# Optimization experiments

Hardware: AMD Instinct MI355X
Metric: run time of the kernel (lower is better)

The kernel has to match this reference:

```python
import jax, jax.numpy as jnp
import numpy as np

B, N, KD, VD, ID, H = 2, 2048, 1024, 1024, 1024, 16
HD = ID // H
SCALE = ID ** (-0.5)  # module quirk: scale uses inner_dim, not head_dim
EPS = 1e-5


def layernorm(x, g, b):
    mu = jnp.mean(x, axis=-1, keepdims=True)
    var = jnp.var(x, axis=-1, keepdims=True)
    return (x - mu) * jax.lax.rsqrt(var + EPS) * g + b


def setup_inputs() -> dict:
    key = jax.random.key(0)
    ks = jax.random.split(key, 12)
    d = {
        "keys": jax.random.normal(ks[0], (B, N, KD), jnp.float32),
        "values": jax.random.normal(ks[1], (B, N, VD), jnp.float32),
        "qk_norm_g": jnp.ones((KD,), jnp.float32),
        "qk_norm_b": jnp.zeros((KD,), jnp.float32),
        "value_norm_g": jnp.ones((VD,), jnp.float32),
        "value_norm_b": jnp.zeros((VD,), jnp.float32),
        "key_norm_g": jnp.ones((ID,), jnp.float32),
        "key_norm_b": jnp.zeros((ID,), jnp.float32),
        "query_norm_g": jnp.ones((ID,), jnp.float32),
        "query_norm_b": jnp.zeros((ID,), jnp.float32),
        "w_qk": jax.random.normal(ks[2], (KD, 2 * ID), jnp.float32) * (KD ** -0.5),
        "w_v": jax.random.normal(ks[3], (VD, ID), jnp.float32) * (VD ** -0.5),
        "w_out": jax.random.normal(ks[4], (ID, VD), jnp.float32) * (ID ** -0.5),
        "b_out": jnp.zeros((VD,), jnp.float32),
    }
    return d


def reference(keys, values, qk_norm_g, qk_norm_b, value_norm_g, value_norm_b,
              key_norm_g, key_norm_b, query_norm_g, query_norm_b,
              w_qk, w_v, w_out, b_out):
    keys = layernorm(keys, qk_norm_g, qk_norm_b)
    values = layernorm(values, value_norm_g, value_norm_b)
    qk = keys @ w_qk  # [B,N,2*ID]
    q, k = qk[..., :ID], qk[..., ID:]
    q = layernorm(q, query_norm_g, query_norm_b)
    k = layernorm(k, key_norm_g, key_norm_b)
    # b n (h d) -> b h n d
    q = q.reshape(B, N, H, HD).transpose(0, 2, 1, 3)
    k = k.reshape(B, N, H, HD).transpose(0, 2, 1, 3)
    v = (values @ w_v).reshape(B, N, H, HD).transpose(0, 2, 1, 3)
    dots = jnp.einsum('bhqd,bhkd->bhqk', q, k) * SCALE
    attn = jax.nn.softmax(dots, axis=-1)
    out = jnp.einsum('bhqk,bhkd->bhqd', attn, v)
    out = out.transpose(0, 2, 1, 3).reshape(B, N, ID)
    return out @ w_out + b_out
```

## Files before the change

kernel.cpp:

```cpp
#include <hip/hip_runtime.h>
#include <hip/hip_bf16.h>
#include <type_traits>


typedef __hip_bfloat16 bf16;
typedef __attribute__((ext_vector_type(8))) short bf16x8;
typedef __attribute__((ext_vector_type(4))) float f32x4;

#define MFMA_BF16(a, b, c) __builtin_amdgcn_mfma_f32_16x16x32_bf16((a), (b), (c), 0, 0, 0)

__device__ __forceinline__ float us2f(unsigned short u) {
  unsigned int v = ((unsigned int)u) << 16;
  return __builtin_bit_cast(float, v);
}

__device__ __forceinline__ unsigned pack_bf16x2(float a, float b) {
  union { __hip_bfloat162 h; unsigned u; } cv;
  cv.h = __float22bfloat162_rn(float2{a, b});
  return cv.u;
}

__device__ __forceinline__ unsigned pack_bf16x2_trunc(float a, float b) {
  return __builtin_amdgcn_perm(__builtin_bit_cast(unsigned, b),
                               __builtin_bit_cast(unsigned, a), 0x07060302u);
}

__device__ __forceinline__ void gl_lds16(const bf16* g, bf16* l) {
  __builtin_amdgcn_global_load_lds(
      (const __attribute__((address_space(1))) void*)g,
      (__attribute__((address_space(3))) void*)l, 16, 0, 0);
}

__device__ __forceinline__ void barrier_pinned() {
  __builtin_amdgcn_s_barrier();
  __builtin_amdgcn_sched_barrier(0);
}

template <typename TIN>
__device__ __forceinline__ void ln_core(
    const TIN* __restrict__ in, const float* __restrict__ gamma,
    const float* __restrict__ beta, bf16* __restrict__ out,
    int stride, int D, float sc, int row, float* red)
{
  const int t = threadIdx.x;
  float x0, x1, x2, x3;
  if constexpr (std::is_same_v<TIN, float>) {
    float4 u = *(const float4*)(in + (size_t)row * stride + t * 4);
    x0 = u.x; x1 = u.y; x2 = u.z; x3 = u.w;
  } else {
    ushort4 u = *(const ushort4*)(in + (size_t)row * stride + t * 4);
    x0 = us2f(u.x); x1 = us2f(u.y); x2 = us2f(u.z); x3 = us2f(u.w);
  }
  float s = x0 + x1 + x2 + x3;
  float s2 = x0 * x0 + x1 * x1 + x2 * x2 + x3 * x3;
#pragma unroll
  for (int m = 1; m < 64; m <<= 1) {
    s += __shfl_xor(s, m);
    s2 += __shfl_xor(s2, m);
  }
  const int w = t >> 6, lane = t & 63;
  if (lane == 0) { red[w] = s; red[4 + w] = s2; }
  __syncthreads();
  if (t == 0) {
    float S = red[0] + red[1] + red[2] + red[3];
    float S2 = red[4] + red[5] + red[6] + red[7];
    float mu = S / (float)D;
    float var = S2 / (float)D - mu * mu;
    red[8] = mu;
    red[9] = rsqrtf(var + 1e-5f);
  }
  __syncthreads();
  const float mu = red[8], rs = red[9];
  float4 g4 = *(const float4*)(gamma + t * 4);
  float4 b4 = *(const float4*)(beta + t * 4);
  uint2 o;
  o.x = pack_bf16x2(((x0 - mu) * rs * g4.x + b4.x) * sc, ((x1 - mu) * rs * g4.y + b4.y) * sc);
  o.y = pack_bf16x2(((x2 - mu) * rs * g4.z + b4.z) * sc, ((x3 - mu) * rs * g4.w + b4.w) * sc);
  *(uint2*)(out + (size_t)row * D + t * 4) = o;
}

template <typename TIN>
__global__ __launch_bounds__(256) void ln2_kernel(
    const TIN* __restrict__ in0, const TIN* __restrict__ in1, int stride,
    const float* __restrict__ g0, const float* __restrict__ b0,
    const float* __restrict__ g1, const float* __restrict__ b1,
    bf16* __restrict__ out0, bf16* __restrict__ out1, int D,
    float sc0, float sc1)
{
  __shared__ float red[10];
  const int which = blockIdx.y;
  ln_core<TIN>(which ? in1 : in0, which ? g1 : g0, which ? b1 : b0,
               which ? out1 : out0, stride, D, which ? sc1 : sc0,
               blockIdx.x, red);
}

__device__ __forceinline__ void transpose_core(
    const float* __restrict__ in, bf16* __restrict__ out, int C,
    int r0, int c0, float (*tile)[68])
{
  const int R = 1024;
  const int t = threadIdx.x;
  const int lr = t >> 2, lc = (t & 3) * 16;
  const float* src = in + (size_t)(r0 + lr) * C + (c0 + lc);
#pragma unroll
  for (int i = 0; i < 4; ++i) {
    float4 u = *(const float4*)(src + i * 4);
    tile[lr][lc + i * 4 + 0] = u.x;
    tile[lr][lc + i * 4 + 1] = u.y;
    tile[lr][lc + i * 4 + 2] = u.z;
    tile[lr][lc + i * 4 + 3] = u.w;
  }
  __syncthreads();
  __align__(16) bf16 tmp[16];
#pragma unroll
  for (int j = 0; j < 16; ++j) tmp[j] = __float2bfloat16(tile[lc + j][lr]);
  bf16* dst = out + (size_t)(c0 + lr) * R + (r0 + lc);
  *(bf16x8*)dst       = *(const bf16x8*)&tmp[0];
  *(bf16x8*)(dst + 8) = *(const bf16x8*)&tmp[8];
}

__global__ __launch_bounds__(256) void prep_kernel(
    const float* __restrict__ keys, const float* __restrict__ values,
    const float* __restrict__ qk_g, const float* __restrict__ qk_b,
    const float* __restrict__ val_g, const float* __restrict__ val_b,
    bf16* __restrict__ keys_ln, bf16* __restrict__ values_ln,
    const float* __restrict__ w_qk, bf16* __restrict__ wqkT,
    const float* __restrict__ w_v, bf16* __restrict__ wvT,
    const float* __restrict__ w_out, bf16* __restrict__ woutT)
{
  __shared__ float tile[64][68];
  __shared__ float red[10];
  const int bid = blockIdx.x;
  if (bid < 8192) {
    const int row = bid >> 1, which = bid & 1;
    ln_core<float>(which ? values : keys, which ? val_g : qk_g,
                   which ? val_b : qk_b, which ? values_ln : keys_ln,
                   1024, 1024, 1.0f, row, red);
  } else {
    const int tz = bid - 8192;
    if (tz < 512) {
      transpose_core(w_qk, wqkT, 2048, (tz >> 5) * 64, (tz & 31) * 64, tile);
    } else if (tz < 768) {
      const int s = tz - 512;
      transpose_core(w_v, wvT, 1024, (s >> 4) * 64, (s & 15) * 64, tile);
    } else {
      const int s = tz - 768;
      transpose_core(w_out, woutT, 1024, (s >> 4) * 64, (s & 15) * 64, tile);
    }
  }
}

template <int BM, int BN, int TMODE, typename TOUT>
__device__ __forceinline__ void gemm_core(
    const bf16* __restrict__ A, const bf16* __restrict__ Bt,
    const float* __restrict__ bias, TOUT* __restrict__ C,
    int N, int K, int has_bias, int bx, int by, bf16* smem)
{
  constexpr int MT = BM / 32, NT = BN / 32;
  constexpr int ASL = BM / 32, BSL = BN / 32;
  constexpr int BUFE = (BM + BN) * 64;
  const int t = threadIdx.x;
  const int w = t >> 6, lane = t & 63, l15 = lane & 15, quad = lane >> 4;
  const int wy = w >> 1, wx = w & 1;
  const bf16* Ab = A + (size_t)by * BM * K;
  const bf16* Bb = Bt + (size_t)bx * BN * K;
  f32x4 acc[MT][NT] = {};

  const bf16* aptr[ASL];
  const bf16* bptr[BSL];
#pragma unroll
  for (int i = 0; i < ASL; ++i) {
    int s = i * 256 + t, row = s >> 3, c = (s & 7) ^ (row & 7);
    aptr[i] = Ab + (size_t)row * K + (c << 3);
  }
#pragma unroll
  for (int i = 0; i < BSL; ++i) {
    int s = i * 256 + t, row = s >> 3, c = (s & 7) ^ (row & 7);
    bptr[i] = Bb + (size_t)row * K + (c << 3);
  }

  auto stage = [&](bf16* buf, int kc) {
#pragma unroll
    for (int i = 0; i < ASL; ++i)
      gl_lds16(aptr[i] + kc, buf + (i * 256 + t) * 8);
#pragma unroll
    for (int i = 0; i < BSL; ++i)
      gl_lds16(bptr[i] + kc, buf + BM * 64 + (i * 256 + t) * 8);
  };

  const int sw = (quad ^ (l15 & 7)) << 3;
  const int NK = K >> 6;

  stage(smem, 0);

  for (int kt = 0; kt < NK; ++kt) {
    const int cur = kt & 1;
    bf16* lA = smem + cur * BUFE;
    bf16* lB = lA + BM * 64;
    barrier_pinned();
    if (kt + 1 < NK) {
      stage(smem + (cur ^ 1) * BUFE, (kt + 1) << 6);
      if constexpr (ASL + BSL == 8)
        asm volatile("s_waitcnt vmcnt(8)" ::: "memory");
      else
        asm volatile("s_waitcnt vmcnt(6)" ::: "memory");
    } else {
      asm volatile("s_waitcnt vmcnt(0)" ::: "memory");
    }
    barrier_pinned();

#pragma unroll
    for (int h = 0; h < 2; ++h) {
      const int so = sw ^ (h << 5);
      bf16x8 af[MT], bfr[NT];
#pragma unroll
      for (int mt = 0; mt < MT; ++mt)
        af[mt] = *(const bf16x8*)&lA[(wy * (BM / 2) + mt * 16 + l15) * 64 + so];
#pragma unroll
      for (int nt = 0; nt < NT; ++nt)
        bfr[nt] = *(const bf16x8*)&lB[(wx * (BN / 2) + nt * 16 + l15) * 64 + so];
#pragma unroll
      for (int mt = 0; mt < MT; ++mt)
#pragma unroll
        for (int nt = 0; nt < NT; ++nt)
          acc[mt][nt] = MFMA_BF16(af[mt], bfr[nt], acc[mt][nt]);
    }
  }

  if constexpr (TMODE == 1) {
    constexpr int STR = BM + 8;
    static_assert(BN * STR <= 2 * BUFE, "lOut must fit staging buffers");
    bf16* lOut = smem;
    __syncthreads();
#pragma unroll
    for (int mt = 0; mt < MT; ++mt)
#pragma unroll
      for (int nt = 0; nt < NT; ++nt) {
        const int d = wx * (BN / 2) + nt * 16 + l15;
        const int n = wy * (BM / 2) + mt * 16 + quad * 4;
        uint2 pk;
        pk.x = pack_bf16x2(acc[mt][nt][0], acc[mt][nt][1]);
        pk.y = pack_bf16x2(acc[mt][nt][2], acc[mt][nt][3]);
        *(uint2*)&lOut[d * STR + n] = pk;
      }
    __syncthreads();
    const int row0 = by * BM;
    const int bidx = row0 >> 11, n0 = row0 & 2047;
    const int col0 = bx * BN;
    constexpr int CPR = BM / 32;
    constexpr int NITER = (BN * CPR) / 256;
#pragma unroll
    for (int it = 0; it < NITER; ++it) {
      const int idx = it * 256 + t;
      const int d = idx / CPR, off = (idx % CPR) * 32;
      const bf16* srcp = &lOut[d * STR + off];
      bf16* g = (bf16*)C + ((size_t)(bidx << 10) + col0 + d) * 2048 + n0 + off;
#pragma unroll
      for (int j = 0; j < 4; ++j)
        *(bf16x8*)(g + j * 8) = *(const bf16x8*)(srcp + j * 8);
    }
  } else {
    const int row_base = by * BM + wy * (BM / 2);
    const int col_base = bx * BN + wx * (BN / 2);
#pragma unroll
    for (int mt = 0; mt < MT; ++mt)
#pragma unroll
      for (int nt = 0; nt < NT; ++nt) {
        const int col = col_base + nt * 16 + l15;
        const float bb = has_bias ? bias[col] : 0.0f;
#pragma unroll
        for (int r = 0; r < 4; ++r) {
          const int row = row_base + mt * 16 + quad * 4 + r;
          float v = acc[mt][nt][r] + bb;
          if constexpr (std::is_same_v<TOUT, bf16>)
            C[(size_t)row * N + col] = __float2bfloat16(v);
          else
            C[(size_t)row * N + col] = v;
        }
      }
  }
}

template <int BM, int BN, int TMODE, typename TOUT>
__global__ __launch_bounds__(256) void gemm_bt_kernel(
    const bf16* __restrict__ A, const bf16* __restrict__ Bt,
    const float* __restrict__ bias, TOUT* __restrict__ C,
    int N, int K, int has_bias)
{
  __shared__ __align__(16) bf16 smem[2 * (BM + BN) * 64];
  gemm_core<BM, BN, TMODE, TOUT>(A, Bt, bias, C, N, K, has_bias,
                                 blockIdx.x, blockIdx.y, smem);
}

__global__ __launch_bounds__(256) void gemm_dual_kernel(
    const bf16* __restrict__ A0, const bf16* __restrict__ B0, bf16* __restrict__ C0,
    const bf16* __restrict__ A1, const bf16* __restrict__ B1, bf16* __restrict__ C1)
{
  __shared__ __align__(16) bf16 smem[2 * 256 * 64];
  const int bid = blockIdx.x;
  if (bid < 512) {
    gemm_core<128, 128, 0, bf16>(A0, B0, nullptr, C0, 2048, 1024, 0,
                                 bid & 15, bid >> 4, smem);
  } else {
    const int b = bid - 512;
    gemm_core<128, 128, 1, bf16>(A1, B1, nullptr, C1, 1024, 1024, 0,
                                 b & 7, b >> 3, smem);
  }
}

__global__ __launch_bounds__(256) void flash_kernel(
    const bf16* __restrict__ Q, const bf16* __restrict__ Km,
    const bf16* __restrict__ Vt, bf16* __restrict__ O)
{
  __shared__ __align__(16) bf16 smem[8192 + 8192 + 8192];
  bf16* lQ = smem;
  bf16* lKb = smem + 8192;
  bf16* lVb = smem + 16384;
  const int t = threadIdx.x;
  const int w = t >> 6, lane = t & 63, l15 = lane & 15, quad = lane >> 4;
  const int qt = blockIdx.x, bh = blockIdx.y;
  const int b = bh >> 4, h = bh & 15;
  const int qrow0 = b * 2048 + qt * 128;
  const bf16* qbase = Q + (size_t)qrow0 * 1024 + h * 64;
  const bf16* kbase = Km + ((size_t)(b * 2048)) * 1024 + h * 64;
  const bf16* vbase = Vt + ((size_t)(b * 1024 + h * 64)) * 2048;

  const int sr0 = t >> 3, sc0 = ((t & 7) ^ (sr0 & 7)) << 3;
  const int sr1 = (256 + t) >> 3, sc1 = (((256 + t) & 7) ^ (sr1 & 7)) << 3;
  const int gr0 = (sr0 & 0x23) | ((sr0 & 0x0C) << 1) | ((sr0 & 0x10) >> 2);
  const int gr1 = (sr1 & 0x23) | ((sr1 & 0x0C) << 1) | ((sr1 & 0x10) >> 2);
  const bf16* kp0 = kbase + gr0 * 1024 + sc0;
  const bf16* kp1 = kbase + gr1 * 1024 + sc1;
  const bf16* vp0 = vbase + sr0 * 2048 + sc0;
  const bf16* vp1 = vbase + sr1 * 2048 + sc1;

#pragma unroll
  for (int i = 0; i < 4; ++i) {
    int s = i * 256 + t;
    int row = s >> 3, c = (s & 7) ^ (row & 7);
    gl_lds16(qbase + (size_t)row * 1024 + (c << 3), lQ + s * 8);
  }
  gl_lds16(kp0, lKb + t * 8);
  gl_lds16(kp1, lKb + (256 + t) * 8);
  gl_lds16(vp0, lVb + t * 8);
  gl_lds16(vp1, lVb + (256 + t) * 8);
  asm volatile("s_waitcnt vmcnt(4)" ::: "memory");
  barrier_pinned();

  const int sw = (quad ^ (l15 & 7)) << 3;
  bf16x8 qf[2][2];
#pragma unroll
  for (int mset = 0; mset < 2; ++mset) {
    const int row = w * 32 + mset * 16 + l15;
    qf[mset][0] = *(const bf16x8*)&lQ[row * 64 + sw];
    qf[mset][1] = *(const bf16x8*)&lQ[row * 64 + (sw ^ 32)];
  }

  f32x4 o_acc[4][2] = {};
  f32x4 l_vec[2] = {};

  for (int kt = 0; kt < 32; ++kt) {
    const int cur = kt & 1;
    bf16* lK = lKb + cur * 4096;
    bf16* lV = lVb + cur * 4096;
    bf16* lKn = lKb + (cur ^ 1) * 4096;
    bf16* lVn = lVb + (cur ^ 1) * 4096;

    barrier_pinned();
    {
      const int ktn = (kt + 1) & 31;
      const int ko = ktn << 16;
      const int vo = ktn << 6;
      gl_lds16(kp0 + ko, lKn + t * 8);
      gl_lds16(kp1 + ko, lKn + (256 + t) * 8);
      gl_lds16(vp0 + vo, lVn + t * 8);
      gl_lds16(vp1 + vo, lVn + (256 + t) * 8);
    }
    asm volatile("s_waitcnt vmcnt(4)" ::: "memory");
    barrier_pinned();

    bf16x8 kf[4][2];
#pragma unroll
    for (int nt = 0; nt < 4; ++nt) {
      kf[nt][0] = *(const bf16x8*)&lK[(nt * 16 + l15) * 64 + sw];
      kf[nt][1] = *(const bf16x8*)&lK[(nt * 16 + l15) * 64 + (sw ^ 32)];
    }

    bf16x8 pa[2][2];
#pragma unroll
    for (int mset = 0; mset < 2; ++mset) {
#pragma unroll
      for (int half = 0; half < 2; ++half) {
        f32x4 z0 = {}, z1 = {};
        z0 = MFMA_BF16(kf[2 * half + 0][0], qf[mset][0], z0);
        z0 = MFMA_BF16(kf[2 * half + 0][1], qf[mset][1], z0);
        z1 = MFMA_BF16(kf[2 * half + 1][0], qf[mset][0], z1);
        z1 = MFMA_BF16(kf[2 * half + 1][1], qf[mset][1], z1);
        f32x4 p0, p1;
#pragma unroll
        for (int r = 0; r < 4; ++r) {
          p0[r] = __builtin_amdgcn_exp2f(z0[r]);
          p1[r] = __builtin_amdgcn_exp2f(z1[r]);
        }
        l_vec[mset] += p0 + p1;
        union { unsigned u[4]; bf16x8 v; } cv;
        cv.u[0] = pack_bf16x2_trunc(p0[0], p0[1]);
        cv.u[1] = pack_bf16x2_trunc(p0[2], p0[3]);
        cv.u[2] = pack_bf16x2_trunc(p1[0], p1[1]);
        cv.u[3] = pack_bf16x2_trunc(p1[2], p1[3]);
        pa[mset][half] = cv.v;
      }
    }

    bf16x8 vf[4][2];
#pragma unroll
    for (int dt = 0; dt < 4; ++dt) {
      vf[dt][0] = *(const bf16x8*)&lV[(dt * 16 + l15) * 64 + sw];
      vf[dt][1] = *(const bf16x8*)&lV[(dt * 16 + l15) * 64 + (sw ^ 32)];
    }

    __builtin_amdgcn_s_setprio(1);
#pragma unroll
    for (int mset = 0; mset < 2; ++mset)
#pragma unroll
      for (int dt = 0; dt < 4; ++dt) {
        o_acc[dt][mset] = MFMA_BF16(vf[dt][0], pa[mset][0], o_acc[dt][mset]);
        o_acc[dt][mset] = MFMA_BF16(vf[dt][1], pa[mset][1], o_acc[dt][mset]);
      }
    __builtin_amdgcn_s_setprio(0);
  }

#pragma unroll
  for (int mset = 0; mset < 2; ++mset) {
    float tsum = l_vec[mset][0] + l_vec[mset][1] + l_vec[mset][2] + l_vec[mset][3];
    tsum += __shfl_xor(tsum, 16);
    tsum += __shfl_xor(tsum, 32);
    const float inv = 1.0f / tsum;
    const int m = qrow0 + w * 32 + mset * 16 + l15;
#pragma unroll
    for (int dt = 0; dt < 4; ++dt) {
      uint2 ok;
      ok.x = pack_bf16x2(o_acc[dt][mset][0] * inv, o_acc[dt][mset][1] * inv);
      ok.y = pack_bf16x2(o_acc[dt][mset][2] * inv, o_acc[dt][mset][3] * inv);
      *(uint2*)&O[(size_t)m * 1024 + h * 64 + dt * 16 + quad * 4] = ok;
    }
  }
}

extern "C" void kernel_launch(void* const* d_in, const int* in_sizes, int n_in,
                              void* d_out, int out_size, void* d_ws, size_t ws_size,
                              hipStream_t stream)
{
  (void)in_sizes; (void)n_in; (void)out_size; (void)ws_size;
  const float* keys   = (const float*)d_in[0];
  const float* values = (const float*)d_in[1];
  const float* qk_g   = (const float*)d_in[2];
  const float* qk_b   = (const float*)d_in[3];
  const float* val_g  = (const float*)d_in[4];
  const float* val_b  = (const float*)d_in[5];
  const float* key_g  = (const float*)d_in[6];
  const float* key_b  = (const float*)d_in[7];
  const float* qry_g  = (const float*)d_in[8];
  const float* qry_b  = (const float*)d_in[9];
  const float* w_qk   = (const float*)d_in[10];
  const float* w_v    = (const float*)d_in[11];
  const float* w_out  = (const float*)d_in[12];
  const float* b_out  = (const float*)d_in[13];
  float* out = (float*)d_out;

  const float CEXP = 0.03125f * 1.44269504f;

  char* ws = (char*)d_ws;
  const size_t MB = 1024 * 1024;
  bf16* keys_ln   = (bf16*)(ws + 0);
  bf16* values_ln = (bf16*)(ws + 8 * MB);
  bf16* qk        = (bf16*)(ws + 16 * MB);
  bf16* vt        = (bf16*)(ws + 32 * MB);
  bf16* qln       = (bf16*)(ws + 0);
  bf16* kln       = (bf16*)(ws + 8 * MB);
  bf16* attn      = (bf16*)(ws + 16 * MB);
  bf16* wqkT      = (bf16*)(ws + 40 * MB);
  bf16* wvT       = (bf16*)(ws + 44 * MB);
  bf16* woutT     = (bf16*)(ws + 46 * MB);

  prep_kernel<<<dim3(9216), 256, 0, stream>>>(
      keys, values, qk_g, qk_b, val_g, val_b, keys_ln, values_ln,
      w_qk, wqkT, w_v, wvT, w_out, woutT);
  gemm_dual_kernel<<<dim3(768), 256, 0, stream>>>(
      keys_ln, wqkT, qk, values_ln, wvT, vt);
  ln2_kernel<bf16><<<dim3(4096, 2), 256, 0, stream>>>(
      qk, qk + 1024, 2048, qry_g, qry_b, key_g, key_b, qln, kln, 1024, CEXP, 1.0f);
  flash_kernel<<<dim3(16, 32), 256, 0, stream>>>(qln, kln, vt, attn);
  gemm_bt_kernel<128, 64, 0, float><<<dim3(16, 32), 256, 0, stream>>>(attn, woutT, b_out, out, 1024, 1024, 1);
}
```

Baseline: 219.5 us.

## Double KV tile per flash iteration and compute softmax row sums via MFMA

The flash attention loop now stages two 64-key K/V sub-tiles per iteration, so a 128-key chunk sits in each LDS buffer. This halves the number of barrier pairs and loop iterations, at the cost of twice the LDS footprint. Row sums of the exponentiated scores are now accumulated by an extra MFMA against a vector of bf16 ones, replacing the VALU adds and the final cross-lane shuffles. Because the sum is taken from the bf16-truncated probabilities, it matches the values actually fed into the P·V product. The extra MFMAs add work on the matrix unit, and the larger LDS use may lower occupancy.

```diff
diff --git a/kernel.cpp b/kernel.cpp
--- a/kernel.cpp
+++ b/kernel.cpp
@@ -312,10 +312,10 @@
     const bf16* __restrict__ Q, const bf16* __restrict__ Km,
     const bf16* __restrict__ Vt, bf16* __restrict__ O)
 {
-  __shared__ __align__(16) bf16 smem[8192 + 8192 + 8192];
+  __shared__ __align__(16) bf16 smem[8192 + 16384 + 16384];
   bf16* lQ = smem;
   bf16* lKb = smem + 8192;
-  bf16* lVb = smem + 16384;
+  bf16* lVb = smem + 8192 + 16384;
   const int t = threadIdx.x;
   const int w = t >> 6, lane = t & 63, l15 = lane & 15, quad = lane >> 4;
   const int qt = blockIdx.x, bh = blockIdx.y;
@@ -334,17 +334,23 @@
   const bf16* vp0 = vbase + sr0 * 2048 + sc0;
   const bf16* vp1 = vbase + sr1 * 2048 + sc1;
 
+  auto stage_kv = [&](bf16* kdst, bf16* vdst, int kro, int vco) {
+    const int ko = kro << 10;
+    gl_lds16(kp0 + ko, kdst + t * 8);
+    gl_lds16(kp1 + ko, kdst + (256 + t) * 8);
+    gl_lds16(vp0 + vco, vdst + t * 8);
+    gl_lds16(vp1 + vco, vdst + (256 + t) * 8);
+  };
+
 #pragma unroll
   for (int i = 0; i < 4; ++i) {
     int s = i * 256 + t;
     int row = s >> 3, c = (s & 7) ^ (row & 7);
     gl_lds16(qbase + (size_t)row * 1024 + (c << 3), lQ + s * 8);
   }
-  gl_lds16(kp0, lKb + t * 8);
-  gl_lds16(kp1, lKb + (256 + t) * 8);
-  gl_lds16(vp0, lVb + t * 8);
-  gl_lds16(vp1, lVb + (256 + t) * 8);
-  asm volatile("s_waitcnt vmcnt(4)" ::: "memory");
+  stage_kv(lKb, lVb, 0, 0);
+  stage_kv(lKb + 4096, lVb + 4096, 64, 64);
+  asm volatile("s_waitcnt vmcnt(8)" ::: "memory");
   barrier_pinned();
 
   const int sw = (quad ^ (l15 & 7)) << 3;
@@ -357,85 +363,90 @@
   }
 
   f32x4 o_acc[4][2] = {};
-  f32x4 l_vec[2] = {};
-
-  for (int kt = 0; kt < 32; ++kt) {
+  f32x4 s_acc[2] = {};
+  const short ONEB = (short)0x3F80;
+  const bf16x8 ones = {ONEB, ONEB, ONEB, ONEB, ONEB, ONEB, ONEB, ONEB};
+
+  for (int kt = 0; kt < 16; ++kt) {
     const int cur = kt & 1;
-    bf16* lK = lKb + cur * 4096;
-    bf16* lV = lVb + cur * 4096;
-    bf16* lKn = lKb + (cur ^ 1) * 4096;
-    bf16* lVn = lVb + (cur ^ 1) * 4096;
+    bf16* lK = lKb + cur * 8192;
+    bf16* lV = lVb + cur * 8192;
+    bf16* lKn = lKb + (cur ^ 1) * 8192;
+    bf16* lVn = lVb + (cur ^ 1) * 8192;
 
     barrier_pinned();
     {
-      const int ktn = (kt + 1) & 31;
-      const int ko = ktn << 16;
-      const int vo = ktn << 6;
-      gl_lds16(kp0 + ko, lKn + t * 8);
-      gl_lds16(kp1 + ko, lKn + (256 + t) * 8);
-      gl_lds16(vp0 + vo, lVn + t * 8);
-      gl_lds16(vp1 + vo, lVn + (256 + t) * 8);
-    }
-    asm volatile("s_waitcnt vmcnt(4)" ::: "memory");
+      const int ktn = (kt + 1) & 15;
+      const int kro = ktn << 7;
+      const int vco = ktn << 7;
+      stage_kv(lKn, lVn, kro, vco);
+      stage_kv(lKn + 4096, lVn + 4096, kro + 64, vco + 64);
+    }
+    asm volatile("s_waitcnt vmcnt(8)" ::: "memory");
     barrier_pinned();
 
-    bf16x8 kf[4][2];
-#pragma unroll
-    for (int nt = 0; nt < 4; ++nt) {
-      kf[nt][0] = *(const bf16x8*)&lK[(nt * 16 + l15) * 64 + sw];
-      kf[nt][1] = *(const bf16x8*)&lK[(nt * 16 + l15) * 64 + (sw ^ 32)];
-    }
-
-    bf16x8 pa[2][2];
-#pragma unroll
-    for (int mset = 0; mset < 2; ++mset) {
-#pragma unroll
-      for (int half = 0; half < 2; ++half) {
-        f32x4 z0 = {}, z1 = {};
-        z0 = MFMA_BF16(kf[2 * half + 0][0], qf[mset][0], z0);
-        z0 = MFMA_BF16(kf[2 * half + 0][1], qf[mset][1], z0);
-        z1 = MFMA_BF16(kf[2 * half + 1][0], qf[mset][0], z1);
-        z1 = MFMA_BF16(kf[2 * half + 1][1], qf[mset][1], z1);
-        f32x4 p0, p1;
-#pragma unroll
-        for (int r = 0; r < 4; ++r) {
-          p0[r] = __builtin_amdgcn_exp2f(z0[r]);
-          p1[r] = __builtin_amdgcn_exp2f(z1[r]);
+#pragma unroll
+    for (int sub = 0; sub < 2; ++sub) {
+      bf16* lKs = lK + sub * 4096;
+      bf16* lVs = lV + sub * 4096;
+
+      bf16x8 kf[4][2];
+#pragma unroll
+      for (int nt = 0; nt < 4; ++nt) {
+        kf[nt][0] = *(const bf16x8*)&lKs[(nt * 16 + l15) * 64 + sw];
+        kf[nt][1] = *(const bf16x8*)&lKs[(nt * 16 + l15) * 64 + (sw ^ 32)];
+      }
+
+      bf16x8 pa[2][2];
+#pragma unroll
+      for (int mset = 0; mset < 2; ++mset) {
+#pragma unroll
+        for (int half = 0; half < 2; ++half) {
+          f32x4 z0 = {}, z1 = {};
+          z0 = MFMA_BF16(kf[2 * half + 0][0], qf[mset][0], z0);
+          z0 = MFMA_BF16(kf[2 * half + 0][1], qf[mset][1], z0);
+          z1 = MFMA_BF16(kf[2 * half + 1][0], qf[mset][0], z1);
+          z1 = MFMA_BF16(kf[2 * half + 1][1], qf[mset][1], z1);
+          f32x4 p0, p1;
+#pragma unroll
+          for (int r = 0; r < 4; ++r) {
+            p0[r] = __builtin_amdgcn_exp2f(z0[r]);
+            p1[r] = __builtin_amdgcn_exp2f(z1[r]);
+          }
+          union { unsigned u[4]; bf16x8 v; } cv;
+          cv.u[0] = pack_bf16x2_trunc(p0[0], p0[1]);
+          cv.u[1] = pack_bf16x2_trunc(p0[2], p0[3]);
+          cv.u[2] = pack_bf16x2_trunc(p1[0], p1[1]);
+          cv.u[3] = pack_bf16x2_trunc(p1[2], p1[3]);
+          pa[mset][half] = cv.v;
         }
-        l_vec[mset] += p0 + p1;
-        union { unsigned u[4]; bf16x8 v; } cv;
-        cv.u[0] = pack_bf16x2_trunc(p0[0], p0[1]);
-        cv.u[1] = pack_bf16x2_trunc(p0[2], p0[3]);
-        cv.u[2] = pack_bf16x2_trunc(p1[0], p1[1]);
-        cv.u[3] = pack_bf16x2_trunc(p1[2], p1[3]);
-        pa[mset][half] = cv.v;
       }
-    }
-
-    bf16x8 vf[4][2];
-#pragma unroll
-    for (int dt = 0; dt < 4; ++dt) {
-      vf[dt][0] = *(const bf16x8*)&lV[(dt * 16 + l15) * 64 + sw];
-      vf[dt][1] = *(const bf16x8*)&lV[(dt * 16 + l15) * 64 + (sw ^ 32)];
-    }
-
-    __builtin_amdgcn_s_setprio(1);
-#pragma unroll
-    for (int mset = 0; mset < 2; ++mset)
+
+      bf16x8 vf[4][2];
 #pragma unroll
       for (int dt = 0; dt < 4; ++dt) {
-        o_acc[dt][mset] = MFMA_BF16(vf[dt][0], pa[mset][0], o_acc[dt][mset]);
-        o_acc[dt][mset] = MFMA_BF16(vf[dt][1], pa[mset][1], o_acc[dt][mset]);
+        vf[dt][0] = *(const bf16x8*)&lVs[(dt * 16 + l15) * 64 + sw];
+        vf[dt][1] = *(const bf16x8*)&lVs[(dt * 16 + l15) * 64 + (sw ^ 32)];
       }
-    __builtin_amdgcn_s_setprio(0);
+
+      __builtin_amdgcn_s_setprio(1);
+#pragma unroll
+      for (int mset = 0; mset < 2; ++mset) {
+        s_acc[mset] = MFMA_BF16(ones, pa[mset][0], s_acc[mset]);
+        s_acc[mset] = MFMA_BF16(ones, pa[mset][1], s_acc[mset]);
+#pragma unroll
+        for (int dt = 0; dt < 4; ++dt) {
+          o_acc[dt][mset] = MFMA_BF16(vf[dt][0], pa[mset][0], o_acc[dt][mset]);
+          o_acc[dt][mset] = MFMA_BF16(vf[dt][1], pa[mset][1], o_acc[dt][mset]);
+        }
+      }
+      __builtin_amdgcn_s_setprio(0);
+    }
   }
 
 #pragma unroll
   for (int mset = 0; mset < 2; ++mset) {
-    float tsum = l_vec[mset][0] + l_vec[mset][1] + l_vec[mset][2] + l_vec[mset][3];
-    tsum += __shfl_xor(tsum, 16);
-    tsum += __shfl_xor(tsum, 32);
-    const float inv = 1.0f / tsum;
+    const float inv = 1.0f / s_acc[mset][0];
     const int m = qrow0 + w * 32 + mset * 16 + l15;
 #pragma unroll
     for (int dt = 0; dt < 4; ++dt) {
```

New measurement: 223.4 us. No clear change (+1.8%).
